# Kernel optimization log

Measured on AMD Instinct MI355X. Metric: run time of the kernel, lower is better.

## Reference

```python
import jax, jax.numpy as jnp
import numpy as np

S, B, H, NH = 2048, 1, 4096, 32
HD = H // NH            # 128
ROT = int(HD * 0.25)    # 32 partial rotary dims
BASE = 10000.0


def setup_inputs() -> dict:
    key = jax.random.key(0)
    ks = jax.random.split(key, 4)
    hidden_states = jax.random.normal(ks[0], (S, B, H), dtype=jnp.float32)
    W_qkv = jax.random.normal(ks[1], (3 * H, H), dtype=jnp.float32) * 0.02
    b_qkv = jnp.zeros((3 * H,), dtype=jnp.float32)
    W_dense = jax.random.normal(ks[2], (H, H), dtype=jnp.float32) * 0.02
    b_dense = jnp.zeros((H,), dtype=jnp.float32)
    # causal left-to-right mask, True = attend
    attention_mask = jnp.tril(jnp.ones((S, S), dtype=bool))[None, None]  # [1,1,S,S]
    return dict(hidden_states=hidden_states, attention_mask=attention_mask,
                W_qkv=W_qkv, b_qkv=b_qkv, W_dense=W_dense, b_dense=b_dense)


def _rotate_half(x):
    x1, x2 = jnp.split(x, 2, axis=-1)
    return jnp.concatenate((-x2, x1), axis=-1)


def reference(hidden_states, attention_mask, W_qkv, b_qkv, W_dense, b_dense):
    S_, B_ = hidden_states.shape[:2]
    qkv = hidden_states @ W_qkv.T + b_qkv                    # [S,B,3H]
    qkv = qkv.reshape(S_, B_, NH, 3 * HD)
    q, k, v = qkv[..., :HD], qkv[..., HD:2 * HD], qkv[..., 2 * HD:]

    # partial rotary embedding (GPT-NeoX style, offset=0, no KV cache)
    inv_freq = 1.0 / (BASE ** (jnp.arange(0, ROT, 2, dtype=jnp.float32) / ROT))
    t = jnp.arange(S_, dtype=jnp.float32)
    freqs = jnp.einsum('s,d->sd', t, inv_freq)               # [S,ROT/2]
    emb = jnp.concatenate((freqs, freqs), axis=-1)           # [S,ROT]
    cos = jnp.cos(emb)[:, None, None, :]                     # [S,1,1,ROT]
    sin = jnp.sin(emb)[:, None, None, :]

    def rope(x):
        return x * cos + _rotate_half(x) * sin

    q = jnp.concatenate((rope(q[..., :ROT]), q[..., ROT:]), axis=-1)
    k = jnp.concatenate((rope(k[..., :ROT]), k[..., ROT:]), axis=-1)

    # scaled dot-product attention with explicit score matrix
    scores = jnp.einsum('sbhd,tbhd->bhst', q, k) / np.float32(np.sqrt(HD))
    scores = jnp.where(attention_mask, scores, jnp.float32(-10000.0))
    probs = jax.nn.softmax(scores, axis=-1)                  # [B,NH,S,S]
    ctx = jnp.einsum('bhst,tbhd->sbhd', probs, v).reshape(S_, B_, H)
    return ctx @ W_dense.T + b_dense                         # [S,B,H]
```

## Files before the change

kernel.cpp:

```cpp
#include <hip/hip_runtime.h>
#include <hip/hip_bf16.h>
#include <math.h>

typedef __bf16 bf16_t;
typedef bf16_t bf16x8 __attribute__((ext_vector_type(8)));
typedef bf16_t bf16x4 __attribute__((ext_vector_type(4)));
typedef float floatx4 __attribute__((ext_vector_type(4)));

#define S_LEN 2048
#define QK_LD 8192

__global__ void convert_all(const float* __restrict__ a, bf16_t* __restrict__ ao,
                            const float* __restrict__ b, bf16_t* __restrict__ bo,
                            const float* __restrict__ c, bf16_t* __restrict__ co) {
    int i = blockIdx.x * 256 + threadIdx.x;
    const float* src; bf16_t* dst; int j;
    if (i < 2097152)        { src = a; dst = ao; j = i; }
    else if (i < 14680064)  { src = b; dst = bo; j = i - 2097152; }
    else                    { src = c; dst = co; j = i - 14680064; }
    float4 v = ((const float4*)src)[j];
    bf16x4 o;
    o.x = (bf16_t)v.x; o.y = (bf16_t)v.y; o.z = (bf16_t)v.z; o.w = (bf16_t)v.w;
    ((bf16x4*)dst)[j] = o;
}

__device__ __forceinline__ void async_copy16(const void* g, void* l) {
    __builtin_amdgcn_global_load_lds(
        (const __attribute__((address_space(1))) unsigned int*)g,
        (__attribute__((address_space(3))) unsigned int*)l, 16, 0, 0);
}

__device__ __forceinline__ void fast_sincos(float x, float* sn, float* cs) {
    float rev = x * 0.15915494309189535f;
    rev = rev - floorf(rev);
    *sn = __builtin_amdgcn_sinf(rev);
    *cs = __builtin_amdgcn_cosf(rev);
}

__global__ __launch_bounds__(512, 2) void qkv_gemm256(
    const bf16_t* __restrict__ A, const bf16_t* __restrict__ B,
    const float* __restrict__ bias, bf16_t* __restrict__ qkout,
    bf16_t* __restrict__ vt)
{
    __shared__ bf16_t lds[65536];
    const int t = threadIdx.x;
    const int lane = t & 63;
    const int w = t >> 6;
    const int l15 = lane & 15, quad = lane >> 4;
    const int wr = w >> 2, wc = w & 3;
    const int bm = blockIdx.x & 7, bn = blockIdx.x >> 3;

    const int srow = t >> 2;
    const int kslot8 = ((t & 3) ^ ((t >> 3) & 3)) << 3;
    const bf16_t* Ag = A + (size_t)(bm * 256 + srow) * 4096 + kslot8;
    const bf16_t* Bg = B + (size_t)(bn * 256 + srow) * 4096 + kslot8;
    bf16_t* ldsW = lds + t * 8;

    const int xorv8 = (quad ^ ((l15 >> 1) & 3)) << 3;
    const bf16_t* pA0 = lds + (wr * 128 + l15) * 32 + xorv8;
    const bf16_t* pB0 = lds + 32768 + (wc * 64 + l15) * 32 + xorv8;

    floatx4 acc[8][4];
    #pragma unroll
    for (int i = 0; i < 8; i++)
        #pragma unroll
        for (int j = 0; j < 4; j++)
            acc[i][j] = (floatx4){0.f, 0.f, 0.f, 0.f};

    bf16x8 a[4], b[4];

#define STAGE_A(tile, kh, dd) do { \
    const bf16_t* g_ = Ag + (tile) * 64 + (kh) * 32; \
    bf16_t* l_ = ldsW + ((dd) * 2 + (kh)) * 8192; \
    async_copy16(g_, l_); \
    async_copy16(g_ + (size_t)128 * 4096, l_ + 4096); \
} while (0)
#define STAGE_B(tile, kh, dd) do { \
    const bf16_t* g_ = Bg + (tile) * 64 + (kh) * 32; \
    bf16_t* l_ = ldsW + 32768 + ((dd) * 2 + (kh)) * 8192; \
    async_copy16(g_, l_); \
    async_copy16(g_ + (size_t)128 * 4096, l_ + 4096); \
} while (0)
#define LOAD_B4(dd, kh) do { \
    const bf16_t* pb_ = pB0 + ((dd) * 2 + (kh)) * 8192; \
    b[0] = *(const bf16x8*)(pb_ + 0 * 512); \
    b[1] = *(const bf16x8*)(pb_ + 1 * 512); \
    b[2] = *(const bf16x8*)(pb_ + 2 * 512); \
    b[3] = *(const bf16x8*)(pb_ + 3 * 512); \
} while (0)
#define LOAD_A4(dd, kh, ph) do { \
    const bf16_t* pa_ = pA0 + ((dd) * 2 + (kh)) * 8192 + (ph) * 2048; \
    a[0] = *(const bf16x8*)(pa_ + 0 * 512); \
    a[1] = *(const bf16x8*)(pa_ + 1 * 512); \
    a[2] = *(const bf16x8*)(pa_ + 2 * 512); \
    a[3] = *(const bf16x8*)(pa_ + 3 * 512); \
} while (0)
#define MFMA16(ph) do { \
    __builtin_amdgcn_s_setprio(1); \
    _Pragma("unroll") \
    for (int mi_ = 0; mi_ < 4; mi_++) \
        _Pragma("unroll") \
        for (int ni_ = 0; ni_ < 4; ni_++) \
            acc[(ph) * 4 + mi_][ni_] = __builtin_amdgcn_mfma_f32_16x16x32_bf16( \
                a[mi_], b[ni_], acc[(ph) * 4 + mi_][ni_], 0, 0, 0); \
    __builtin_amdgcn_s_setprio(0); \
} while (0)
#define PH_MID() do { \
    __builtin_amdgcn_sched_barrier(0); \
    __builtin_amdgcn_s_barrier(); \
    asm volatile("s_waitcnt lgkmcnt(0)" ::: "memory"); \
    __builtin_amdgcn_sched_barrier(0); \
} while (0)
#define PH_END() do { \
    __builtin_amdgcn_sched_barrier(0); \
    asm volatile("" ::: "memory"); \
    __builtin_amdgcn_s_barrier(); \
} while (0)

    STAGE_A(0, 0, 0); STAGE_B(0, 0, 0);
    STAGE_A(0, 1, 0); STAGE_B(0, 1, 0);
    STAGE_A(1, 0, 1); STAGE_B(1, 0, 1);
    asm volatile("s_waitcnt vmcnt(8)" ::: "memory");
    __builtin_amdgcn_s_barrier();

    for (int tt = 0; tt < 64; tt += 2) {
        LOAD_B4(0, 0); LOAD_A4(0, 0, 0);
        STAGE_A(tt + 1, 1, 1);
        PH_MID(); MFMA16(0); PH_END();

        LOAD_A4(0, 0, 1);
        STAGE_B(tt + 1, 1, 1);
        PH_MID(); MFMA16(1);
        asm volatile("s_waitcnt vmcnt(8)" ::: "memory");
        PH_END();

        LOAD_B4(0, 1); LOAD_A4(0, 1, 0);
        if (tt + 2 < 64) STAGE_A(tt + 2, 0, 0);
        PH_MID(); MFMA16(0); PH_END();

        LOAD_A4(0, 1, 1);
        if (tt + 2 < 64) STAGE_B(tt + 2, 0, 0);
        PH_MID(); MFMA16(1);
        if (tt + 2 < 64) { asm volatile("s_waitcnt vmcnt(8)" ::: "memory"); }
        else             { asm volatile("s_waitcnt vmcnt(4)" ::: "memory"); }
        PH_END();

        LOAD_B4(1, 0); LOAD_A4(1, 0, 0);
        if (tt + 2 < 64) STAGE_A(tt + 2, 1, 0);
        PH_MID(); MFMA16(0); PH_END();

        LOAD_A4(1, 0, 1);
        if (tt + 2 < 64) STAGE_B(tt + 2, 1, 0);
        PH_MID(); MFMA16(1);
        if (tt + 2 < 64) { asm volatile("s_waitcnt vmcnt(8)" ::: "memory"); }
        else             { asm volatile("s_waitcnt vmcnt(0)" ::: "memory"); }
        PH_END();

        LOAD_B4(1, 1); LOAD_A4(1, 1, 0);
        if (tt + 3 < 64) STAGE_A(tt + 3, 0, 1);
        PH_MID(); MFMA16(0); PH_END();

        LOAD_A4(1, 1, 1);
        if (tt + 3 < 64) STAGE_B(tt + 3, 0, 1);
        PH_MID(); MFMA16(1);
        if (tt + 3 < 64) { asm volatile("s_waitcnt vmcnt(8)" ::: "memory"); }
        PH_END();
    }

#undef STAGE_A
#undef STAGE_B
#undef LOAD_B4
#undef LOAD_A4
#undef MFMA16
#undef PH_MID
#undef PH_END

    const int colbase = bn * 256 + wc * 64;
    #pragma unroll
    for (int ni = 0; ni < 4; ni++) {
        const int cb = colbase + ni * 16;
        const float bv = bias[cb + l15];
        const int h = cb / 384;
        const int rem = cb - h * 384;
        if (rem < 256) {
            bf16_t* qb = qkout + (size_t)h * 256 + rem + l15;
            #pragma unroll
            for (int mi = 0; mi < 8; mi++) {
                const int row0 = bm * 256 + wr * 128 + mi * 16 + quad * 4;
                #pragma unroll
                for (int r = 0; r < 4; r++)
                    qb[(size_t)(row0 + r) * QK_LD] = (bf16_t)(acc[mi][ni][r] + bv);
            }
        } else {
            const int d0 = rem - 256 + l15;
            bf16_t* vb = vt + ((size_t)h * 128 + d0) * S_LEN;
            #pragma unroll
            for (int mi = 0; mi < 8; mi++) {
                const int row0 = bm * 256 + wr * 128 + mi * 16 + quad * 4;
                bf16x4 pv;
                #pragma unroll
                for (int r = 0; r < 4; r++) pv[r] = (bf16_t)(acc[mi][ni][r] + bv);
                *(bf16x4*)&vb[row0] = pv;
            }
        }
    }
}

__global__ void rope_kernel(bf16_t* __restrict__ qk) {
    int idx = blockIdx.x * 256 + threadIdx.x;
    int j = idx & 15;
    int h = (idx >> 4) & 31;
    int s = idx >> 9;
    float invf = exp2f(-(float)j * 0.8304820237218405f);
    float sn, cs;
    fast_sincos((float)s * invf, &sn, &cs);
    bf16_t* base = qk + (size_t)s * QK_LD + h * 256;
    {
        float x1 = (float)base[j], x2 = (float)base[j + 16];
        base[j]      = (bf16_t)(x1 * cs - x2 * sn);
        base[j + 16] = (bf16_t)(x2 * cs + x1 * sn);
    }
    {
        bf16_t* kb = base + 128;
        float x1 = (float)kb[j], x2 = (float)kb[j + 16];
        kb[j]      = (bf16_t)(x1 * cs - x2 * sn);
        kb[j + 16] = (bf16_t)(x2 * cs + x1 * sn);
    }
}

__global__ __launch_bounds__(256) void dense_gemm(
    const bf16_t* __restrict__ A, const bf16_t* __restrict__ B,
    const float* __restrict__ bias, float* __restrict__ C,
    int M, int N, int K)
{
    __shared__ bf16_t As[64 * 32];
    __shared__ bf16_t Bs[128 * 32];
    const int t    = threadIdx.x;
    const int lane = t & 63;
    const int w    = t >> 6;
    const int l15  = lane & 15;
    const int quad = lane >> 4;
    const int bm = blockIdx.y, bn = blockIdx.x;
    const int mw = (w >> 1) * 32, nw = (w & 1) * 64;

    floatx4 acc[2][4];
    #pragma unroll
    for (int i = 0; i < 2; i++)
        #pragma unroll
        for (int j = 0; j < 4; j++)
            acc[i][j] = (floatx4){0.f, 0.f, 0.f, 0.f};

    const int r0 = t >> 2;
    const int c0 = (t & 3) * 8;
    const bf16_t* Aptr = A + (size_t)(bm * 64 + r0) * K + c0;
    const bf16_t* Bptr = B + (size_t)(bn * 128 + r0) * K + c0;
    bf16_t* AsW = As + t * 8;
    bf16_t* BsW = Bs + t * 8;

    for (int k0 = 0; k0 < K; k0 += 32) {
        __syncthreads();
        async_copy16(Aptr + k0, AsW);
        async_copy16(Bptr + k0, BsW);
        async_copy16(Bptr + k0 + (size_t)64 * K, BsW + 2048);
        __syncthreads();

        bf16x8 a[2], b[4];
        #pragma unroll
        for (int mi = 0; mi < 2; mi++)
            a[mi] = *(const bf16x8*)&As[(mw + mi * 16 + l15) * 32 + quad * 8];
        #pragma unroll
        for (int ni = 0; ni < 4; ni++)
            b[ni] = *(const bf16x8*)&Bs[(nw + ni * 16 + l15) * 32 + quad * 8];
        #pragma unroll
        for (int mi = 0; mi < 2; mi++)
            #pragma unroll
            for (int ni = 0; ni < 4; ni++)
                acc[mi][ni] = __builtin_amdgcn_mfma_f32_16x16x32_bf16(a[mi], b[ni], acc[mi][ni], 0, 0, 0);
    }

    #pragma unroll
    for (int ni = 0; ni < 4; ni++) {
        int col = bn * 128 + nw + ni * 16 + l15;
        float bv = bias[col];
        #pragma unroll
        for (int mi = 0; mi < 2; mi++)
            #pragma unroll
            for (int r = 0; r < 4; r++) {
                int row = bm * 64 + mw + mi * 16 + quad * 4 + r;
                C[(size_t)row * N + col] = acc[mi][ni][r] + bv;
            }
    }
}

#define QK_LDS 136
#define V_LDS  72
__global__ __launch_bounds__(256) void flash_attn(
    const bf16_t* __restrict__ qk, const bf16_t* __restrict__ Vt,
    bf16_t* __restrict__ ctx)
{
    __shared__ bf16_t Qs[64 * QK_LDS];
    __shared__ bf16_t Ks[64 * QK_LDS];
    __shared__ bf16_t Vs[128 * V_LDS];
    __shared__ bf16_t Ps[64 * V_LDS];
    const int h = blockIdx.y;
    const int qb = (int)gridDim.x - 1 - blockIdx.x;
    const int t = threadIdx.x;
    const int w = t >> 6, lane = t & 63;
    const int quad = lane >> 4, l15 = lane & 15;
    const float SCL = 0.08838834764831845f * 1.4426950408889634f;

    {
        const bf16_t* qbase = qk + (size_t)(qb * 64) * QK_LD + h * 256;
        int rr = t >> 4, cc = (t & 15) * 8;
        #pragma unroll
        for (int p = 0; p < 4; p++) {
            int row = rr + p * 16;
            *(bf16x8*)&Qs[row * QK_LDS + cc] = *(const bf16x8*)&qbase[(size_t)row * QK_LD + cc];
        }
    }

    floatx4 o[8];
    #pragma unroll
    for (int i = 0; i < 8; i++) o[i] = (floatx4){0.f, 0.f, 0.f, 0.f};
    float lsum[4] = {0.f, 0.f, 0.f, 0.f};

    for (int kt = 0; kt <= qb; kt++) {
        __syncthreads();
        {
            const bf16_t* kbase = qk + (size_t)(kt * 64) * QK_LD + h * 256 + 128;
            int rr = t >> 4, cc = (t & 15) * 8;
            #pragma unroll
            for (int p = 0; p < 4; p++) {
                int row = rr + p * 16;
                *(bf16x8*)&Ks[row * QK_LDS + cc] = *(const bf16x8*)&kbase[(size_t)row * QK_LD + cc];
            }
            const bf16_t* vbase = Vt + (size_t)h * 128 * S_LEN + kt * 64;
            int vr = t >> 3, vc = (t & 7) * 8;
            #pragma unroll
            for (int p = 0; p < 4; p++) {
                int row = vr + p * 32;
                *(bf16x8*)&Vs[row * V_LDS + vc] = *(const bf16x8*)&vbase[(size_t)row * S_LEN + vc];
            }
        }
        __syncthreads();

        floatx4 sacc[4];
        #pragma unroll
        for (int ni = 0; ni < 4; ni++) sacc[ni] = (floatx4){0.f, 0.f, 0.f, 0.f};
        #pragma unroll
        for (int ks = 0; ks < 4; ks++) {
            bf16x8 aq = *(const bf16x8*)&Qs[(w * 16 + l15) * QK_LDS + ks * 32 + quad * 8];
            #pragma unroll
            for (int ni = 0; ni < 4; ni++) {
                bf16x8 bk = *(const bf16x8*)&Ks[(ni * 16 + l15) * QK_LDS + ks * 32 + quad * 8];
                sacc[ni] = __builtin_amdgcn_mfma_f32_16x16x32_bf16(aq, bk, sacc[ni], 0, 0, 0);
            }
        }

        float pv[4][4];
        #pragma unroll
        for (int ni = 0; ni < 4; ni++)
            #pragma unroll
            for (int r = 0; r < 4; r++)
                pv[ni][r] = __builtin_amdgcn_exp2f(sacc[ni][r] * SCL);
        if (kt == qb) {
            #pragma unroll
            for (int ni = 0; ni < 4; ni++) {
                int key = ni * 16 + l15;
                #pragma unroll
                for (int r = 0; r < 4; r++)
                    if (key > w * 16 + quad * 4 + r) pv[ni][r] = 0.f;
            }
        }
        #pragma unroll
        for (int ni = 0; ni < 4; ni++)
            #pragma unroll
            for (int r = 0; r < 4; r++) {
                lsum[r] += pv[ni][r];
                Ps[(w * 16 + quad * 4 + r) * V_LDS + ni * 16 + l15] = (bf16_t)pv[ni][r];
            }
        asm volatile("s_waitcnt lgkmcnt(0)" ::: "memory");

        #pragma unroll
        for (int ks = 0; ks < 2; ks++) {
            bf16x8 ap = *(const bf16x8*)&Ps[(w * 16 + l15) * V_LDS + ks * 32 + quad * 8];
            #pragma unroll
            for (int ni = 0; ni < 8; ni++) {
                bf16x8 bv = *(const bf16x8*)&Vs[(ni * 16 + l15) * V_LDS + ks * 32 + quad * 8];
                o[ni] = __builtin_amdgcn_mfma_f32_16x16x32_bf16(ap, bv, o[ni], 0, 0, 0);
            }
        }
    }

    float invl[4];
    #pragma unroll
    for (int r = 0; r < 4; r++) {
        float s = lsum[r];
        #pragma unroll
        for (int off = 1; off < 16; off <<= 1)
            s += __shfl_xor(s, off, 16);
        invl[r] = 1.f / s;
    }
    bf16_t* cbase = ctx + (size_t)(qb * 64) * 4096 + h * 128;
    #pragma unroll
    for (int ni = 0; ni < 8; ni++) {
        int col = ni * 16 + l15;
        #pragma unroll
        for (int r = 0; r < 4; r++) {
            int row = w * 16 + quad * 4 + r;
            cbase[(size_t)row * 4096 + col] = (bf16_t)(o[ni][r] * invl[r]);
        }
    }
}

extern "C" void kernel_launch(void* const* d_in, const int* in_sizes, int n_in,
                              void* d_out, int out_size, void* d_ws, size_t ws_size,
                              hipStream_t stream) {
    const float* hidden = (const float*)d_in[0];
    const float* Wqkv   = (const float*)d_in[2];
    const float* bqkv   = (const float*)d_in[3];
    const float* Wd     = (const float*)d_in[4];
    const float* bd     = (const float*)d_in[5];
    float* out = (float*)d_out;

    char* ws = (char*)d_ws;
    bf16_t* h_bf    = (bf16_t*)(ws);
    bf16_t* wqkv_bf = (bf16_t*)(ws + 16777216);
    bf16_t* wd_bf   = (bf16_t*)(ws + 117440512);
    bf16_t* qk      = (bf16_t*)(ws + 150994944);
    bf16_t* vt      = (bf16_t*)(ws + 184549376);
    bf16_t* ctx     = (bf16_t*)(ws + 201326592);

    convert_all<<<73728, 256, 0, stream>>>(hidden, h_bf, Wqkv, wqkv_bf, Wd, wd_bf);
    qkv_gemm256<<<dim3(384), 512, 0, stream>>>(h_bf, wqkv_bf, bqkv, qk, vt);
    rope_kernel<<<4096, 256, 0, stream>>>(qk);
    flash_attn<<<dim3(32, 32), 256, 0, stream>>>(qk, vt, ctx);
    dense_gemm<<<dim3(32, 32), 256, 0, stream>>>(ctx, wd_bf, bd, out, 2048, 4096, 4096);
}
```

Before: 817.1 us.

## Enlarge dense GEMM tile, swizzle block order, prefetch K/V in attention

The dense projection GEMM moves to 128x128 tiles on a 1D grid, with a block mapping that groups N-tiles per XCD so blocks sharing operands run near each other. The QKV GEMM gets a similar XCD-aware remapping of block indices. Flash attention now loads the next K/V tile into registers while the current one is computed, and raises wave priority around the MFMA sections. Together these aim to cut global-memory traffic, improve L2 locality and hide load latency, at the cost of more registers and fewer blocks for the dense GEMM.

```diff
diff --git a/kernel.cpp b/kernel.cpp
--- a/kernel.cpp
+++ b/kernel.cpp
@@ -48,7 +48,10 @@
     const int w = t >> 6;
     const int l15 = lane & 15, quad = lane >> 4;
     const int wr = w >> 2, wc = w & 3;
-    const int bm = blockIdx.x & 7, bn = blockIdx.x >> 3;
+    const int x = blockIdx.x & 7;
+    const int j = blockIdx.x >> 3;
+    const int bm = j / 6;
+    const int bn = x * 6 + (j % 6);
 
     const int srow = t >> 2;
     const int kslot8 = ((t & 3) ^ ((t >> 3) & 3)) << 3;
@@ -64,8 +67,8 @@
     #pragma unroll
     for (int i = 0; i < 8; i++)
         #pragma unroll
-        for (int j = 0; j < 4; j++)
-            acc[i][j] = (floatx4){0.f, 0.f, 0.f, 0.f};
+        for (int jj = 0; jj < 4; jj++)
+            acc[i][jj] = (floatx4){0.f, 0.f, 0.f, 0.f};
 
     bf16x8 a[4], b[4];
 
@@ -228,31 +231,34 @@
     }
 }
 
-__global__ __launch_bounds__(256) void dense_gemm(
+__global__ __launch_bounds__(256) void dense_gemm128(
     const bf16_t* __restrict__ A, const bf16_t* __restrict__ B,
-    const float* __restrict__ bias, float* __restrict__ C,
-    int M, int N, int K)
+    const float* __restrict__ bias, float* __restrict__ C)
 {
-    __shared__ bf16_t As[64 * 32];
+    const int K = 4096, N = 4096;
+    __shared__ bf16_t As[128 * 32];
     __shared__ bf16_t Bs[128 * 32];
     const int t    = threadIdx.x;
     const int lane = t & 63;
     const int w    = t >> 6;
     const int l15  = lane & 15;
     const int quad = lane >> 4;
-    const int bm = blockIdx.y, bn = blockIdx.x;
-    const int mw = (w >> 1) * 32, nw = (w & 1) * 64;
-
-    floatx4 acc[2][4];
-    #pragma unroll
-    for (int i = 0; i < 2; i++)
-        #pragma unroll
-        for (int j = 0; j < 4; j++)
-            acc[i][j] = (floatx4){0.f, 0.f, 0.f, 0.f};
+    const int x = blockIdx.x & 7;
+    const int j = blockIdx.x >> 3;
+    const int bn = x * 4 + (j & 3);
+    const int bm = j >> 2;
+    const int mw = (w >> 1) * 64, nw = (w & 1) * 64;
+
+    floatx4 acc[4][4];
+    #pragma unroll
+    for (int i = 0; i < 4; i++)
+        #pragma unroll
+        for (int jj = 0; jj < 4; jj++)
+            acc[i][jj] = (floatx4){0.f, 0.f, 0.f, 0.f};
 
     const int r0 = t >> 2;
     const int c0 = (t & 3) * 8;
-    const bf16_t* Aptr = A + (size_t)(bm * 64 + r0) * K + c0;
+    const bf16_t* Aptr = A + (size_t)(bm * 128 + r0) * K + c0;
     const bf16_t* Bptr = B + (size_t)(bn * 128 + r0) * K + c0;
     bf16_t* AsW = As + t * 8;
     bf16_t* BsW = Bs + t * 8;
@@ -260,19 +266,20 @@
     for (int k0 = 0; k0 < K; k0 += 32) {
         __syncthreads();
         async_copy16(Aptr + k0, AsW);
+        async_copy16(Aptr + k0 + (size_t)64 * K, AsW + 2048);
         async_copy16(Bptr + k0, BsW);
         async_copy16(Bptr + k0 + (size_t)64 * K, BsW + 2048);
         __syncthreads();
 
-        bf16x8 a[2], b[4];
-        #pragma unroll
-        for (int mi = 0; mi < 2; mi++)
+        bf16x8 a[4], b[4];
+        #pragma unroll
+        for (int mi = 0; mi < 4; mi++)
             a[mi] = *(const bf16x8*)&As[(mw + mi * 16 + l15) * 32 + quad * 8];
         #pragma unroll
         for (int ni = 0; ni < 4; ni++)
             b[ni] = *(const bf16x8*)&Bs[(nw + ni * 16 + l15) * 32 + quad * 8];
         #pragma unroll
-        for (int mi = 0; mi < 2; mi++)
+        for (int mi = 0; mi < 4; mi++)
             #pragma unroll
             for (int ni = 0; ni < 4; ni++)
                 acc[mi][ni] = __builtin_amdgcn_mfma_f32_16x16x32_bf16(a[mi], b[ni], acc[mi][ni], 0, 0, 0);
@@ -283,10 +290,10 @@
         int col = bn * 128 + nw + ni * 16 + l15;
         float bv = bias[col];
         #pragma unroll
-        for (int mi = 0; mi < 2; mi++)
+        for (int mi = 0; mi < 4; mi++)
             #pragma unroll
             for (int r = 0; r < 4; r++) {
-                int row = bm * 64 + mw + mi * 16 + quad * 4 + r;
+                int row = bm * 128 + mw + mi * 16 + quad * 4 + r;
                 C[(size_t)row * N + col] = acc[mi][ni][r] + bv;
             }
     }
@@ -309,9 +316,11 @@
     const int quad = lane >> 4, l15 = lane & 15;
     const float SCL = 0.08838834764831845f * 1.4426950408889634f;
 
+    const int rr = t >> 4, cc = (t & 15) * 8;
+    const int vr = t >> 3, vc = (t & 7) * 8;
+
     {
         const bf16_t* qbase = qk + (size_t)(qb * 64) * QK_LD + h * 256;
-        int rr = t >> 4, cc = (t & 15) * 8;
         #pragma unroll
         for (int p = 0; p < 4; p++) {
             int row = rr + p * 16;
@@ -319,34 +328,40 @@
         }
     }
 
+    bf16x8 kreg[4], vreg[4];
+#define LOAD_KV(kt_) do { \
+    const bf16_t* kb_ = qk + (size_t)((kt_) * 64) * QK_LD + h * 256 + 128; \
+    _Pragma("unroll") \
+    for (int p = 0; p < 4; p++) \
+        kreg[p] = *(const bf16x8*)&kb_[(size_t)(rr + p * 16) * QK_LD + cc]; \
+    const bf16_t* vb_ = Vt + (size_t)h * 128 * S_LEN + (kt_) * 64; \
+    _Pragma("unroll") \
+    for (int p = 0; p < 4; p++) \
+        vreg[p] = *(const bf16x8*)&vb_[(size_t)(vr + p * 32) * S_LEN + vc]; \
+} while (0)
+
     floatx4 o[8];
     #pragma unroll
     for (int i = 0; i < 8; i++) o[i] = (floatx4){0.f, 0.f, 0.f, 0.f};
     float lsum[4] = {0.f, 0.f, 0.f, 0.f};
 
+    LOAD_KV(0);
+
     for (int kt = 0; kt <= qb; kt++) {
         __syncthreads();
-        {
-            const bf16_t* kbase = qk + (size_t)(kt * 64) * QK_LD + h * 256 + 128;
-            int rr = t >> 4, cc = (t & 15) * 8;
-            #pragma unroll
-            for (int p = 0; p < 4; p++) {
-                int row = rr + p * 16;
-                *(bf16x8*)&Ks[row * QK_LDS + cc] = *(const bf16x8*)&kbase[(size_t)row * QK_LD + cc];
-            }
-            const bf16_t* vbase = Vt + (size_t)h * 128 * S_LEN + kt * 64;
-            int vr = t >> 3, vc = (t & 7) * 8;
-            #pragma unroll
-            for (int p = 0; p < 4; p++) {
-                int row = vr + p * 32;
-                *(bf16x8*)&Vs[row * V_LDS + vc] = *(const bf16x8*)&vbase[(size_t)row * S_LEN + vc];
-            }
-        }
+        #pragma unroll
+        for (int p = 0; p < 4; p++)
+            *(bf16x8*)&Ks[(rr + p * 16) * QK_LDS + cc] = kreg[p];
+        #pragma unroll
+        for (int p = 0; p < 4; p++)
+            *(bf16x8*)&Vs[(vr + p * 32) * V_LDS + vc] = vreg[p];
         __syncthreads();
+        if (kt < qb) LOAD_KV(kt + 1);
 
         floatx4 sacc[4];
         #pragma unroll
         for (int ni = 0; ni < 4; ni++) sacc[ni] = (floatx4){0.f, 0.f, 0.f, 0.f};
+        __builtin_amdgcn_s_setprio(1);
         #pragma unroll
         for (int ks = 0; ks < 4; ks++) {
             bf16x8 aq = *(const bf16x8*)&Qs[(w * 16 + l15) * QK_LDS + ks * 32 + quad * 8];
@@ -356,6 +371,7 @@
                 sacc[ni] = __builtin_amdgcn_mfma_f32_16x16x32_bf16(aq, bk, sacc[ni], 0, 0, 0);
             }
         }
+        __builtin_amdgcn_s_setprio(0);
 
         float pv[4][4];
         #pragma unroll
@@ -381,6 +397,7 @@
             }
         asm volatile("s_waitcnt lgkmcnt(0)" ::: "memory");
 
+        __builtin_amdgcn_s_setprio(1);
         #pragma unroll
         for (int ks = 0; ks < 2; ks++) {
             bf16x8 ap = *(const bf16x8*)&Ps[(w * 16 + l15) * V_LDS + ks * 32 + quad * 8];
@@ -390,7 +407,9 @@
                 o[ni] = __builtin_amdgcn_mfma_f32_16x16x32_bf16(ap, bv, o[ni], 0, 0, 0);
             }
         }
-    }
+        __builtin_amdgcn_s_setprio(0);
+    }
+#undef LOAD_KV
 
     float invl[4];
     #pragma unroll
@@ -435,5 +454,5 @@
     qkv_gemm256<<<dim3(384), 512, 0, stream>>>(h_bf, wqkv_bf, bqkv, qk, vt);
     rope_kernel<<<4096, 256, 0, stream>>>(qk);
     flash_attn<<<dim3(32, 32), 256, 0, stream>>>(qk, vt, ctx);
-    dense_gemm<<<dim3(32, 32), 256, 0, stream>>>(ctx, wd_bf, bd, out, 2048, 4096, 4096);
-}
+    dense_gemm128<<<dim3(512), 256, 0, stream>>>(ctx, wd_bf, bd, out);
+}
```

New measurement: 794.3 us. 1.03x faster.
